# Kernel tuning notes

Hardware: AMD Instinct MI355X
Metric: run time of the kernel (lower is better)

The kernel has to match this reference:

```python
import jax, jax.numpy as jnp
import numpy as np

N_SENT, N_DOC, G = 100000, 10000, 32

def _seg_mean_right(x, src, dst, n_dst):
    # DGL GraphConv(norm='right'): sum incoming messages / in_degree (clamped to 1)
    m = jax.ops.segment_sum(x[src], dst, num_segments=n_dst)
    deg = jax.ops.segment_sum(jnp.ones_like(dst, dtype=x.dtype), dst, num_segments=n_dst)
    return m / jnp.maximum(deg, 1.0)[:, None]

def _rel_layer(xs, xd, coeff, basis, loop_w, bias,
               src_ss, dst_ss, src_sd, dst_sd, src_ds, dst_ds):
    # WeightBasis: per-relation weight = sum_b coeff[r,b] * basis[b]
    W = jnp.einsum('rb,bio->rio', coeff, basis)  # [3, in, out]
    # rel 0: sent->doc, rel 1: doc->sent, rel 2: sent->sent; HeteroGraphConv sums per dst ntype
    h_doc = _seg_mean_right(xs, src_sd, dst_sd, N_DOC) @ W[0]
    h_sent = (_seg_mean_right(xd, src_ds, dst_ds, N_SENT) @ W[1]
              + _seg_mean_right(xs, src_ss, dst_ss, N_SENT) @ W[2])
    h_sent = jax.nn.relu(h_sent + xs @ loop_w + bias)
    h_doc = jax.nn.relu(h_doc + xd @ loop_w + bias)
    return h_sent, h_doc

def setup_inputs() -> dict:
    key = jax.random.key(0)
    ks = jax.random.split(key, 20)
    d_in, d_h, d_o = 768, 256, 128
    inp = {
        'x_sent': jax.random.normal(ks[0], (N_SENT, d_in), jnp.float32),
        'x_doc': jax.random.normal(ks[1], (N_DOC, d_in), jnp.float32),
        'coeff1': jax.random.normal(ks[2], (3, 2), jnp.float32),
        'basis1': jax.random.normal(ks[3], (2, d_in, d_h), jnp.float32) * 0.02,
        'loop_w1': jax.random.normal(ks[4], (d_in, d_h), jnp.float32) * 0.02,
        'bias1': jnp.zeros((d_h,), jnp.float32),
        'coeff2': jax.random.normal(ks[5], (3, 2), jnp.float32),
        'basis2': jax.random.normal(ks[6], (2, d_h, d_o), jnp.float32) * 0.05,
        'loop_w2': jax.random.normal(ks[7], (d_h, d_o), jnp.float32) * 0.05,
        'bias2': jnp.zeros((d_o,), jnp.float32),
        'w_score': jax.random.normal(ks[8], (d_o, 1), jnp.float32) * 0.05,
        'b_score': jnp.zeros((1,), jnp.float32),
        'src_ss': jax.random.randint(ks[9], (400000,), 0, N_SENT, jnp.int32),
        'dst_ss': jax.random.randint(ks[10], (400000,), 0, N_SENT, jnp.int32),
        'src_sd': jax.random.randint(ks[11], (100000,), 0, N_SENT, jnp.int32),
        'dst_sd': jax.random.randint(ks[12], (100000,), 0, N_DOC, jnp.int32),
        'src_ds': jax.random.randint(ks[13], (100000,), 0, N_DOC, jnp.int32),
        'dst_ds': jax.random.randint(ks[14], (100000,), 0, N_SENT, jnp.int32),
        'gid_sent': jnp.sort(jax.random.randint(ks[15], (N_SENT,), 0, G, jnp.int32)),
        'gid_doc': jnp.sort(jax.random.randint(ks[16], (N_DOC,), 0, G, jnp.int32)),
        'num_graphs': G,
    }
    return inp

def reference(x_sent, x_doc, coeff1, basis1, loop_w1, bias1,
              coeff2, basis2, loop_w2, bias2, w_score, b_score,
              src_ss, dst_ss, src_sd, dst_sd, src_ds, dst_ds,
              gid_sent, gid_doc, num_graphs):
    h_s, h_d = _rel_layer(x_sent, x_doc, coeff1, basis1, loop_w1, bias1,
                          src_ss, dst_ss, src_sd, dst_sd, src_ds, dst_ds)
    h_s, h_d = _rel_layer(h_s, h_d, coeff2, basis2, loop_w2, bias2,
                          src_ss, dst_ss, src_sd, dst_sd, src_ds, dst_ds)
    # dgl.sum_nodes over batched graph, summed across ntypes
    readout = (jax.ops.segment_sum(h_s, gid_sent, num_segments=num_graphs)
               + jax.ops.segment_sum(h_d, gid_doc, num_segments=num_graphs))
    return readout @ w_score + b_score  # [G, 1]
```

## Files before the change

kernel.cpp:

```cpp
#include <hip/hip_runtime.h>

#define CDIV(a,b) (((a)+(b)-1)/(b))

typedef __attribute__((ext_vector_type(8))) short bf16x8;
typedef __attribute__((ext_vector_type(4))) float floatx4;

__device__ __forceinline__ ushort f2bf(float x) {
    unsigned u = __float_as_uint(x);
    return (ushort)((u + 0x7fffu + ((u >> 16) & 1u)) >> 16);
}
__device__ __forceinline__ float bflo(unsigned v) { return __uint_as_float(v << 16); }
__device__ __forceinline__ float bfhi(unsigned v) { return __uint_as_float(v & 0xffff0000u); }

__device__ __forceinline__ void load_lds16(const ushort* g, ushort* l) {
    __builtin_amdgcn_global_load_lds(
        (const __attribute__((address_space(1))) void*)g,
        (__attribute__((address_space(3))) void*)l, 16, 0, 0);
}


__global__ void zero_f4(float4* __restrict__ p, long long n4) {
    long long i = blockIdx.x * 256LL + threadIdx.x;
    if (i < n4) p[i] = make_float4(0.f, 0.f, 0.f, 0.f);
}

__global__ void fill_w5(ushort* __restrict__ BsT, ushort* __restrict__ BdT,
                        const float* __restrict__ basis, const float* __restrict__ loopw,
                        const float* __restrict__ coeff, int K, int N, long long KN) {
    long long i = blockIdx.x * 256LL + threadIdx.x;
    if (i >= KN) return;
    int k = (int)(i % K), n = (int)(i / K);
    int sec = blockIdx.y;
    float val;
    if (sec == 2 || sec == 4) {
        val = loopw[(size_t)k * N + n];
    } else {
        int r = (sec == 0) ? 0 : (sec == 1) ? 2 : 1;
        val = coeff[2 * r] * basis[(size_t)k * N + n] + coeff[2 * r + 1] * basis[KN + (size_t)k * N + n];
    }
    ushort* dst = (sec < 3) ? BsT : BdT;
    int col0 = (sec == 0) ? 0 : (sec == 1) ? N : (sec == 2) ? 2 * N : (sec == 3) ? 0 : N;
    dst[(size_t)(col0 + n) * K + k] = f2bf(val);
}


__global__ void accum_deg_all(const int* __restrict__ dss, const int* __restrict__ dds,
                              const int* __restrict__ dsd, int nss, int nds, int nsd,
                              int NS, int* __restrict__ deg) {
    int i = blockIdx.x * 256 + threadIdx.x;
    if (i < nss) atomicAdd(&deg[dss[i]], 1);
    else if (i < nss + nds) atomicAdd(&deg[NS + dds[i - nss]], 1);
    else if (i < nss + nds + nsd) atomicAdd(&deg[2 * NS + dsd[i - nss - nds]], 1);
}

__global__ void scan_p1(const int* __restrict__ deg, int n, int* __restrict__ bsum) {
    __shared__ int sd[256];
    int blk = blockIdx.x, tid = threadIdx.x;
    int i0 = blk * 1024 + tid * 4;
    int s = 0;
#pragma unroll
    for (int j = 0; j < 4; ++j) if (i0 + j < n) s += deg[i0 + j];
    sd[tid] = s; __syncthreads();
    for (int o = 128; o; o >>= 1) {
        if (tid < o) sd[tid] += sd[tid + o];
        __syncthreads();
    }
    if (tid == 0) bsum[blk] = sd[0];
}

__global__ void scan_p2(int* __restrict__ bsum, int nb, int* __restrict__ rowptr, int ntot, int etot) {
    __shared__ int sd[256];
    int tid = threadIdx.x;
    int v = (tid < nb) ? bsum[tid] : 0;
    sd[tid] = v; __syncthreads();
    for (int o = 1; o < 256; o <<= 1) {
        int t = (tid >= o) ? sd[tid - o] : 0;
        __syncthreads();
        sd[tid] += t;
        __syncthreads();
    }
    if (tid < nb) bsum[tid] = sd[tid] - v;
    if (tid == 0) rowptr[ntot] = etot;
}

__global__ void scan_p3(const int* __restrict__ deg, int n, const int* __restrict__ bsum,
                        int* __restrict__ rowptr) {
    __shared__ int sd[256];
    int blk = blockIdx.x, tid = threadIdx.x;
    int i0 = blk * 1024 + tid * 4;
    int v[4]; int s = 0;
#pragma unroll
    for (int j = 0; j < 4; ++j) { v[j] = (i0 + j < n) ? deg[i0 + j] : 0; s += v[j]; }
    sd[tid] = s; __syncthreads();
    for (int o = 1; o < 256; o <<= 1) {
        int t = (tid >= o) ? sd[tid - o] : 0;
        __syncthreads();
        sd[tid] += t;
        __syncthreads();
    }
    int excl = bsum[blk] + sd[tid] - s;
#pragma unroll
    for (int j = 0; j < 4; ++j) {
        if (i0 + j < n) rowptr[i0 + j] = excl;
        excl += v[j];
    }
}

__global__ void fill_csr_all(const int* __restrict__ sss, const int* __restrict__ dss,
                             const int* __restrict__ sds, const int* __restrict__ dds,
                             const int* __restrict__ ssd, const int* __restrict__ dsd,
                             int nss, int nds, int nsd, int NS,
                             const int* __restrict__ rowptr, int* __restrict__ fill,
                             int* __restrict__ col) {
    int i = blockIdx.x * 256 + threadIdx.x;
    int d, s;
    if (i < nss) { d = dss[i]; s = sss[i]; }
    else if (i < nss + nds) { int j = i - nss; d = NS + dds[j]; s = sds[j]; }
    else if (i < nss + nds + nsd) { int j = i - nss - nds; d = 2 * NS + dsd[j]; s = ssd[j]; }
    else return;
    int p = rowptr[d] + atomicAdd(&fill[d], 1);
    col[p] = s;
}

template<bool AF32>
__global__ __launch_bounds__(256) void gemm_any(
    const void* __restrict__ Araw, const ushort* __restrict__ Bt, ushort* __restrict__ C,
    int M, int K, int N, int BNX) {
    const int nwg = gridDim.x;
    const int orig = blockIdx.x;
    const int q = nwg >> 3, r = nwg & 7;
    const int xcd = orig & 7, idx = orig >> 3;
    const int wg = (xcd < r ? xcd * (q + 1) : r * (q + 1) + (xcd - r) * q) + idx;
    const int bn = (wg % BNX) * 128;
    const long long bm = (long long)(wg / BNX) * 128LL;

    __shared__ ushort As[128 * 32];
    __shared__ ushort Bs[128 * 32];
    const int tid = threadIdx.x;
    const int lane = tid & 63, wave = tid >> 6;
    const int mo = (wave & 1) * 64, no = (wave >> 1) * 64;
    const int l15 = lane & 15, quad = lane >> 4;
    const int srow0 = wave * 16 + (lane >> 2);
    const int schunk = (lane & 3) * 8;
    floatx4 acc[4][4] = {};

    for (int k0 = 0; k0 < K; k0 += 32) {
#pragma unroll
        for (int t = 0; t < 2; ++t) {
            int row = t * 64 + srow0;
            long long ar = bm + row; if (ar >= M) ar = M - 1;
            if (AF32) {
                const float* A = (const float*)Araw;
                const float* ap = A + ar * (size_t)K + k0 + schunk;
                float4 a0 = *(const float4*)ap;
                float4 a1 = *(const float4*)(ap + 4);
                uint4 o;
                o.x = (unsigned)f2bf(a0.x) | ((unsigned)f2bf(a0.y) << 16);
                o.y = (unsigned)f2bf(a0.z) | ((unsigned)f2bf(a0.w) << 16);
                o.z = (unsigned)f2bf(a1.x) | ((unsigned)f2bf(a1.y) << 16);
                o.w = (unsigned)f2bf(a1.z) | ((unsigned)f2bf(a1.w) << 16);
                *(uint4*)(As + t * 2048 + wave * 512 + lane * 8) = o;
            } else {
                load_lds16((const ushort*)Araw + ar * (size_t)K + k0 + schunk,
                           As + t * 2048 + wave * 512);
            }
            load_lds16(Bt + (size_t)(bn + row) * K + k0 + schunk, Bs + t * 2048 + wave * 512);
        }
        __syncthreads();
        bf16x8 af[4], bfr[4];
#pragma unroll
        for (int mt = 0; mt < 4; ++mt)
            af[mt] = *(const bf16x8*)(As + (mo + mt * 16 + l15) * 32 + quad * 8);
#pragma unroll
        for (int nt = 0; nt < 4; ++nt)
            bfr[nt] = *(const bf16x8*)(Bs + (no + nt * 16 + l15) * 32 + quad * 8);
#pragma unroll
        for (int mt = 0; mt < 4; ++mt)
#pragma unroll
            for (int nt = 0; nt < 4; ++nt)
                acc[mt][nt] = __builtin_amdgcn_mfma_f32_16x16x32_bf16(af[mt], bfr[nt], acc[mt][nt], 0, 0, 0);
        __syncthreads();
    }
#pragma unroll
    for (int mt = 0; mt < 4; ++mt)
#pragma unroll
        for (int i = 0; i < 4; ++i) {
            long long row = bm + mo + mt * 16 + quad * 4 + i;
            if (row < M) {
#pragma unroll
                for (int nt = 0; nt < 4; ++nt)
                    C[row * (size_t)N + bn + no + nt * 16 + l15] = f2bf(acc[mt][nt][i]);
            }
        }
}


__global__ __launch_bounds__(256) void gather_l1(
    const ushort* __restrict__ ys, const ushort* __restrict__ yd,
    const int* __restrict__ rowptr, const int* __restrict__ col,
    const float* __restrict__ bias, ushort* __restrict__ h1s, ushort* __restrict__ h1d,
    int NS, int ND) {
    int d = blockIdx.x * 4 + (threadIdx.x >> 6);
    int lane = threadIdx.x & 63;
    int cb = lane * 4;
    float b0 = bias[cb], b1 = bias[cb + 1], b2 = bias[cb + 2], b3 = bias[cb + 3];
    if (d < NS) {
        float a0 = 0, a1 = 0, a2 = 0, a3 = 0;
        int s0 = rowptr[d], s1 = rowptr[d + 1];
        int e = s0;
        for (; e + 4 <= s1; e += 4) {
            int sA = col[e], sB = col[e + 1], sC = col[e + 2], sD = col[e + 3];
            uint2 vA = *(const uint2*)(ys + (size_t)sA * 768 + 256 + cb);
            uint2 vB = *(const uint2*)(ys + (size_t)sB * 768 + 256 + cb);
            uint2 vC = *(const uint2*)(ys + (size_t)sC * 768 + 256 + cb);
            uint2 vD = *(const uint2*)(ys + (size_t)sD * 768 + 256 + cb);
            a0 += bflo(vA.x) + bflo(vB.x) + bflo(vC.x) + bflo(vD.x);
            a1 += bfhi(vA.x) + bfhi(vB.x) + bfhi(vC.x) + bfhi(vD.x);
            a2 += bflo(vA.y) + bflo(vB.y) + bflo(vC.y) + bflo(vD.y);
            a3 += bfhi(vA.y) + bfhi(vB.y) + bfhi(vC.y) + bfhi(vD.y);
        }
        for (; e < s1; ++e) {
            int s = col[e];
            uint2 v = *(const uint2*)(ys + (size_t)s * 768 + 256 + cb);
            a0 += bflo(v.x); a1 += bfhi(v.x); a2 += bflo(v.y); a3 += bfhi(v.y);
        }
        float inv = 1.f / (float)max(s1 - s0, 1);
        float m0 = a0 * inv, m1 = a1 * inv, m2 = a2 * inv, m3 = a3 * inv;
        a0 = a1 = a2 = a3 = 0.f;
        int t0 = rowptr[NS + d], t1 = rowptr[NS + d + 1];
        for (e = t0; e < t1; ++e) {
            int s = col[e];
            uint2 v = *(const uint2*)(yd + (size_t)s * 512 + cb);
            a0 += bflo(v.x); a1 += bfhi(v.x); a2 += bflo(v.y); a3 += bfhi(v.y);
        }
        inv = 1.f / (float)max(t1 - t0, 1);
        uint2 lv = *(const uint2*)(ys + (size_t)d * 768 + 512 + cb);
        float h0 = fmaxf(m0 + a0 * inv + bflo(lv.x) + b0, 0.f);
        float h1 = fmaxf(m1 + a1 * inv + bfhi(lv.x) + b1, 0.f);
        float h2 = fmaxf(m2 + a2 * inv + bflo(lv.y) + b2, 0.f);
        float h3 = fmaxf(m3 + a3 * inv + bfhi(lv.y) + b3, 0.f);
        uint2 o;
        o.x = (unsigned)f2bf(h0) | ((unsigned)f2bf(h1) << 16);
        o.y = (unsigned)f2bf(h2) | ((unsigned)f2bf(h3) << 16);
        *(uint2*)(h1s + (size_t)d * 256 + cb) = o;
    } else if (d < NS + ND) {
        int dd = d - NS;
        float a0 = 0, a1 = 0, a2 = 0, a3 = 0;
        int s0 = rowptr[2 * NS + dd], s1 = rowptr[2 * NS + dd + 1];
        int e = s0;
        for (; e + 4 <= s1; e += 4) {
            int sA = col[e], sB = col[e + 1], sC = col[e + 2], sD = col[e + 3];
            uint2 vA = *(const uint2*)(ys + (size_t)sA * 768 + cb);
            uint2 vB = *(const uint2*)(ys + (size_t)sB * 768 + cb);
            uint2 vC = *(const uint2*)(ys + (size_t)sC * 768 + cb);
            uint2 vD = *(const uint2*)(ys + (size_t)sD * 768 + cb);
            a0 += bflo(vA.x) + bflo(vB.x) + bflo(vC.x) + bflo(vD.x);
            a1 += bfhi(vA.x) + bfhi(vB.x) + bfhi(vC.x) + bfhi(vD.x);
            a2 += bflo(vA.y) + bflo(vB.y) + bflo(vC.y) + bflo(vD.y);
            a3 += bfhi(vA.y) + bfhi(vB.y) + bfhi(vC.y) + bfhi(vD.y);
        }
        for (; e < s1; ++e) {
            int s = col[e];
            uint2 v = *(const uint2*)(ys + (size_t)s * 768 + cb);
            a0 += bflo(v.x); a1 += bfhi(v.x); a2 += bflo(v.y); a3 += bfhi(v.y);
        }
        float inv = 1.f / (float)max(s1 - s0, 1);
        uint2 lv = *(const uint2*)(yd + (size_t)dd * 512 + 256 + cb);
        float h0 = fmaxf(a0 * inv + bflo(lv.x) + b0, 0.f);
        float h1 = fmaxf(a1 * inv + bfhi(lv.x) + b1, 0.f);
        float h2 = fmaxf(a2 * inv + bflo(lv.y) + b2, 0.f);
        float h3 = fmaxf(a3 * inv + bfhi(lv.y) + b3, 0.f);
        uint2 o;
        o.x = (unsigned)f2bf(h0) | ((unsigned)f2bf(h1) << 16);
        o.y = (unsigned)f2bf(h2) | ((unsigned)f2bf(h3) << 16);
        *(uint2*)(h1d + (size_t)dd * 256 + cb) = o;
    }
}

__global__ __launch_bounds__(256) void gather_l2(
    const ushort* __restrict__ ys, const ushort* __restrict__ yd,
    const int* __restrict__ rowptr, const int* __restrict__ col,
    const float* __restrict__ bias, const float* __restrict__ w,
    const int* __restrict__ gid_s, const int* __restrict__ gid_d,
    float* __restrict__ out, int NS, int ND, int G) {
    __shared__ float part[4][32];
    const int tid = threadIdx.x;
    const int lane = tid & 63, wv = tid >> 6;
    const int cb = lane * 2;
    const float w0 = w[cb], w1 = w[cb + 1];
    const float b0 = bias[cb], b1 = bias[cb + 1];
    float racc = 0.f;
    const int nw = gridDim.x * 4;
    for (int d = blockIdx.x * 4 + wv; d < NS + ND; d += nw) {
        float h0, h1; int g;
        if (d < NS) {
            float a0 = 0.f, a1 = 0.f;
            int s0 = rowptr[d], s1 = rowptr[d + 1];
            int e = s0;
            for (; e + 4 <= s1; e += 4) {
                int sA = col[e], sB = col[e + 1], sC = col[e + 2], sD = col[e + 3];
                unsigned vA = *(const unsigned*)(ys + (size_t)sA * 384 + 128 + cb);
                unsigned vB = *(const unsigned*)(ys + (size_t)sB * 384 + 128 + cb);
                unsigned vC = *(const unsigned*)(ys + (size_t)sC * 384 + 128 + cb);
                unsigned vD = *(const unsigned*)(ys + (size_t)sD * 384 + 128 + cb);
                a0 += bflo(vA) + bflo(vB) + bflo(vC) + bflo(vD);
                a1 += bfhi(vA) + bfhi(vB) + bfhi(vC) + bfhi(vD);
            }
            for (; e < s1; ++e) {
                int s = col[e];
                unsigned v = *(const unsigned*)(ys + (size_t)s * 384 + 128 + cb);
                a0 += bflo(v); a1 += bfhi(v);
            }
            float inv = 1.f / (float)max(s1 - s0, 1);
            float m0 = a0 * inv, m1 = a1 * inv;
            a0 = 0.f; a1 = 0.f;
            int t0 = rowptr[NS + d], t1 = rowptr[NS + d + 1];
            for (e = t0; e < t1; ++e) {
                int s = col[e];
                unsigned v = *(const unsigned*)(yd + (size_t)s * 256 + cb);
                a0 += bflo(v); a1 += bfhi(v);
            }
            inv = 1.f / (float)max(t1 - t0, 1);
            unsigned lv = *(const unsigned*)(ys + (size_t)d * 384 + 256 + cb);
            h0 = fmaxf(m0 + a0 * inv + bflo(lv) + b0, 0.f);
            h1 = fmaxf(m1 + a1 * inv + bfhi(lv) + b1, 0.f);
            g = gid_s[d];
        } else {
            int dd = d - NS;
            float a0 = 0.f, a1 = 0.f;
            int s0 = rowptr[2 * NS + dd], s1 = rowptr[2 * NS + dd + 1];
            int e = s0;
            for (; e + 4 <= s1; e += 4) {
                int sA = col[e], sB = col[e + 1], sC = col[e + 2], sD = col[e + 3];
                unsigned vA = *(const unsigned*)(ys + (size_t)sA * 384 + cb);
                unsigned vB = *(const unsigned*)(ys + (size_t)sB * 384 + cb);
                unsigned vC = *(const unsigned*)(ys + (size_t)sC * 384 + cb);
                unsigned vD = *(const unsigned*)(ys + (size_t)sD * 384 + cb);
                a0 += bflo(vA) + bflo(vB) + bflo(vC) + bflo(vD);
                a1 += bfhi(vA) + bfhi(vB) + bfhi(vC) + bfhi(vD);
            }
            for (; e < s1; ++e) {
                int s = col[e];
                unsigned v = *(const unsigned*)(ys + (size_t)s * 384 + cb);
                a0 += bflo(v); a1 += bfhi(v);
            }
            float inv = 1.f / (float)max(s1 - s0, 1);
            unsigned lv = *(const unsigned*)(yd + (size_t)dd * 256 + 128 + cb);
            h0 = fmaxf(a0 * inv + bflo(lv) + b0, 0.f);
            h1 = fmaxf(a1 * inv + bfhi(lv) + b1, 0.f);
            g = gid_d[dd];
        }
        float sc = h0 * w0 + h1 * w1;
#pragma unroll
        for (int o = 32; o; o >>= 1) sc += __shfl_down(sc, o);
        sc = __shfl(sc, 0);
        if (lane == g) racc += sc;
    }
    if (lane < 32) part[wv][lane] = racc;
    __syncthreads();
    if (tid < G) atomicAdd(&out[tid], part[0][tid] + part[1][tid] + part[2][tid] + part[3][tid]);
}

__global__ void init_out(float* __restrict__ out, const float* __restrict__ b, int G) {
    int i = threadIdx.x;
    if (i < G) out[i] = b[0];
}


extern "C" void kernel_launch(void* const* d_in, const int* in_sizes, int n_in,
                              void* d_out, int out_size, void* d_ws, size_t ws_size,
                              hipStream_t stream) {
    const float* x_sent = (const float*)d_in[0];
    const float* x_doc  = (const float*)d_in[1];
    const float* coeff1 = (const float*)d_in[2];
    const float* basis1 = (const float*)d_in[3];
    const float* loopw1 = (const float*)d_in[4];
    const float* bias1  = (const float*)d_in[5];
    const float* coeff2 = (const float*)d_in[6];
    const float* basis2 = (const float*)d_in[7];
    const float* loopw2 = (const float*)d_in[8];
    const float* bias2  = (const float*)d_in[9];
    const float* wscore = (const float*)d_in[10];
    const float* bscore = (const float*)d_in[11];
    const int* src_ss = (const int*)d_in[12];
    const int* dst_ss = (const int*)d_in[13];
    const int* src_sd = (const int*)d_in[14];
    const int* dst_sd = (const int*)d_in[15];
    const int* src_ds = (const int*)d_in[16];
    const int* dst_ds = (const int*)d_in[17];
    const int* gid_sent = (const int*)d_in[18];
    const int* gid_doc  = (const int*)d_in[19];

    const int DIN = 768, DH = 256, DOo = 128;
    const int NS = in_sizes[0] / DIN;
    const int ND = in_sizes[1] / DIN;
    const int E_SS = in_sizes[12], E_SD = in_sizes[14], E_DS = in_sizes[16];
    const int NTOT = NS + NS + ND;
    const int ETOT = E_SS + E_DS + E_SD;
    const int G = out_size;
    float* out = (float*)d_out;

    char* base = (char*)d_ws;
    size_t off = 0;
    auto alloc = [&](size_t bytes) -> char* {
        char* p = base + off;
        off = (off + bytes + 255) & ~(size_t)255;
        return p;
    };
    ushort* B1sT = (ushort*)alloc((size_t)768 * 768 * 2);
    ushort* B1dT = (ushort*)alloc((size_t)512 * 768 * 2);
    ushort* B2sT = (ushort*)alloc((size_t)384 * 256 * 2);
    ushort* B2dT = (ushort*)alloc((size_t)256 * 256 * 2);
    ushort* ys1 = (ushort*)alloc((size_t)NS * 768 * 2);
    ushort* yd1 = (ushort*)alloc((size_t)ND * 512 * 2);
    ushort* h1s = (ushort*)alloc((size_t)NS * 256 * 2);
    ushort* h1d = (ushort*)alloc((size_t)ND * 256 * 2);
    ushort* ys2 = (ushort*)alloc((size_t)NS * 384 * 2);
    ushort* yd2 = (ushort*)alloc((size_t)ND * 256 * 2);
    int* deg  = (int*)alloc((size_t)2 * NTOT * 4);
    int* fill = deg + NTOT;
    int* rowptr = (int*)alloc((size_t)(NTOT + 1) * 4);
    int* bsum = (int*)alloc(256 * 4);
    int* colall = (int*)alloc((size_t)ETOT * 4);

    long long t1 = (long long)768 * DH, t2 = (long long)256 * DOo;
    fill_w5<<<dim3((unsigned)CDIV(t1, 256), 5), 256, 0, stream>>>(B1sT, B1dT, basis1, loopw1, coeff1, 768, DH, t1);
    fill_w5<<<dim3((unsigned)CDIV(t2, 256), 5), 256, 0, stream>>>(B2sT, B2dT, basis2, loopw2, coeff2, 256, DOo, t2);

    zero_f4<<<(int)CDIV(2 * NTOT / 4, 256), 256, 0, stream>>>((float4*)deg, 2 * NTOT / 4);
    accum_deg_all<<<CDIV(ETOT, 256), 256, 0, stream>>>(dst_ss, dst_ds, dst_sd, E_SS, E_DS, E_SD, NS, deg);
    int nb = CDIV(NTOT, 1024);
    scan_p1<<<nb, 256, 0, stream>>>(deg, NTOT, bsum);
    scan_p2<<<1, 256, 0, stream>>>(bsum, nb, rowptr, NTOT, ETOT);
    scan_p3<<<nb, 256, 0, stream>>>(deg, NTOT, bsum, rowptr);
    fill_csr_all<<<CDIV(ETOT, 256), 256, 0, stream>>>(src_ss, dst_ss, src_ds, dst_ds, src_sd, dst_sd,
                                                      E_SS, E_DS, E_SD, NS, rowptr, fill, colall);

    {
        int mb = CDIV(NS, 128), mb0 = mb / 2;
        int M0 = mb0 * 128;
        gemm_any<true><<<6 * mb0, 256, 0, stream>>>(x_sent, B1sT, ys1, M0, 768, 768, 6);
        gemm_any<true><<<6 * (mb - mb0), 256, 0, stream>>>(
            x_sent + (size_t)M0 * 768, B1sT, ys1 + (size_t)M0 * 768, NS - M0, 768, 768, 6);
    }
    gemm_any<true><<<4 * CDIV(ND, 128), 256, 0, stream>>>(x_doc, B1dT, yd1, ND, 768, 512, 4);

    gather_l1<<<CDIV(NS + ND, 4), 256, 0, stream>>>(ys1, yd1, rowptr, colall, bias1, h1s, h1d, NS, ND);

    gemm_any<false><<<3 * CDIV(NS, 128), 256, 0, stream>>>(h1s, B2sT, ys2, NS, 256, 384, 3);
    gemm_any<false><<<2 * CDIV(ND, 128), 256, 0, stream>>>(h1d, B2dT, yd2, ND, 256, 256, 2);

    init_out<<<1, 64, 0, stream>>>(out, bscore, G);
    gather_l2<<<1100, 256, 0, stream>>>(ys2, yd2, rowptr, colall, bias2, wscore,
                                        gid_sent, gid_doc, out, NS, ND, G);
}
```

Baseline: 1.011 ms.

## Double-buffer LDS tiles in GEMM to overlap global loads with MFMA

Splits the GEMM's A and B shared-memory tiles into two buffers and prefetches the next K-slice while the MFMAs run on the current one. For fp32 A inputs, the next slice is held in registers and converted to bf16 into the alternate buffer after the compute step. This cuts one barrier per iteration and hides global-load latency. In exchange it doubles LDS use and adds prefetch registers, which may lower occupancy.

After: 1.045 ms. 3.4% more time.

```diff
diff --git a/kernel.cpp b/kernel.cpp
--- a/kernel.cpp
+++ b/kernel.cpp
@@ -134,8 +134,8 @@
     const int bn = (wg % BNX) * 128;
     const long long bm = (long long)(wg / BNX) * 128LL;
 
-    __shared__ ushort As[128 * 32];
-    __shared__ ushort Bs[128 * 32];
+    __shared__ ushort As[2][128 * 32];
+    __shared__ ushort Bs[2][128 * 32];
     const int tid = threadIdx.x;
     const int lane = tid & 63, wave = tid >> 6;
     const int mo = (wave & 1) * 64, no = (wave >> 1) * 64;
@@ -143,43 +143,75 @@
     const int srow0 = wave * 16 + (lane >> 2);
     const int schunk = (lane & 3) * 8;
     floatx4 acc[4][4] = {};
-
-    for (int k0 = 0; k0 < K; k0 += 32) {
+    float4 pre[2][2];
+
+    auto stageB = [&](int k0, int buf) {
+#pragma unroll
+        for (int t = 0; t < 2; ++t) {
+            int row = t * 64 + srow0;
+            load_lds16(Bt + (size_t)(bn + row) * K + k0 + schunk,
+                       Bs[buf] + t * 2048 + wave * 512);
+        }
+    };
+    auto stageA_bf16 = [&](int k0, int buf) {
 #pragma unroll
         for (int t = 0; t < 2; ++t) {
             int row = t * 64 + srow0;
             long long ar = bm + row; if (ar >= M) ar = M - 1;
-            if (AF32) {
-                const float* A = (const float*)Araw;
-                const float* ap = A + ar * (size_t)K + k0 + schunk;
-                float4 a0 = *(const float4*)ap;
-                float4 a1 = *(const float4*)(ap + 4);
-                uint4 o;
-                o.x = (unsigned)f2bf(a0.x) | ((unsigned)f2bf(a0.y) << 16);
-                o.y = (unsigned)f2bf(a0.z) | ((unsigned)f2bf(a0.w) << 16);
-                o.z = (unsigned)f2bf(a1.x) | ((unsigned)f2bf(a1.y) << 16);
-                o.w = (unsigned)f2bf(a1.z) | ((unsigned)f2bf(a1.w) << 16);
-                *(uint4*)(As + t * 2048 + wave * 512 + lane * 8) = o;
-            } else {
-                load_lds16((const ushort*)Araw + ar * (size_t)K + k0 + schunk,
-                           As + t * 2048 + wave * 512);
-            }
-            load_lds16(Bt + (size_t)(bn + row) * K + k0 + schunk, Bs + t * 2048 + wave * 512);
-        }
-        __syncthreads();
+            load_lds16((const ushort*)Araw + ar * (size_t)K + k0 + schunk,
+                       As[buf] + t * 2048 + wave * 512);
+        }
+    };
+    auto loadA_f32 = [&](int k0) {
+#pragma unroll
+        for (int t = 0; t < 2; ++t) {
+            int row = t * 64 + srow0;
+            long long ar = bm + row; if (ar >= M) ar = M - 1;
+            const float* ap = (const float*)Araw + ar * (size_t)K + k0 + schunk;
+            pre[t][0] = *(const float4*)ap;
+            pre[t][1] = *(const float4*)(ap + 4);
+        }
+    };
+    auto writeA = [&](int buf) {
+#pragma unroll
+        for (int t = 0; t < 2; ++t) {
+            uint4 o;
+            o.x = (unsigned)f2bf(pre[t][0].x) | ((unsigned)f2bf(pre[t][0].y) << 16);
+            o.y = (unsigned)f2bf(pre[t][0].z) | ((unsigned)f2bf(pre[t][0].w) << 16);
+            o.z = (unsigned)f2bf(pre[t][1].x) | ((unsigned)f2bf(pre[t][1].y) << 16);
+            o.w = (unsigned)f2bf(pre[t][1].z) | ((unsigned)f2bf(pre[t][1].w) << 16);
+            *(uint4*)(As[buf] + t * 2048 + wave * 512 + lane * 8) = o;
+        }
+    };
+
+    if (AF32) { loadA_f32(0); writeA(0); } else { stageA_bf16(0, 0); }
+    stageB(0, 0);
+    __syncthreads();
+
+    int cur = 0;
+    for (int k0 = 0; k0 < K; k0 += 32) {
+        const int nxt = k0 + 32;
+        const bool has = nxt < K;
+        if (has) {
+            if (AF32) loadA_f32(nxt);
+            else      stageA_bf16(nxt, cur ^ 1);
+            stageB(nxt, cur ^ 1);
+        }
         bf16x8 af[4], bfr[4];
 #pragma unroll
         for (int mt = 0; mt < 4; ++mt)
-            af[mt] = *(const bf16x8*)(As + (mo + mt * 16 + l15) * 32 + quad * 8);
+            af[mt] = *(const bf16x8*)(As[cur] + (mo + mt * 16 + l15) * 32 + quad * 8);
 #pragma unroll
         for (int nt = 0; nt < 4; ++nt)
-            bfr[nt] = *(const bf16x8*)(Bs + (no + nt * 16 + l15) * 32 + quad * 8);
+            bfr[nt] = *(const bf16x8*)(Bs[cur] + (no + nt * 16 + l15) * 32 + quad * 8);
 #pragma unroll
         for (int mt = 0; mt < 4; ++mt)
 #pragma unroll
             for (int nt = 0; nt < 4; ++nt)
                 acc[mt][nt] = __builtin_amdgcn_mfma_f32_16x16x32_bf16(af[mt], bfr[nt], acc[mt][nt], 0, 0, 0);
-        __syncthreads();
+        if (has && AF32) writeA(cur ^ 1);
+        __syncthreads();
+        cur ^= 1;
     }
 #pragma unroll
     for (int mt = 0; mt < 4; ++mt)
```

## Use BK=64 GEMM tiles with XOR-swizzled LDS layout pre-applied in global buffers

Applied to the files above, without the earlier changes.

The GEMM K-step grows from 32 to 64, and the shared-memory tiles use an XOR swizzle on 8-element chunks, keyed by row, to avoid LDS bank conflicts on the MFMA fragment reads. Because global_load_lds copies rows linearly, the swizzle is applied when the data is produced: the weight fill kernel and the layer-1 gather outputs write in swizzled order. The fp32 A path now issues all its global loads before converting them to bf16. This halves the barrier count per K and cuts bank conflicts, at the cost of double the LDS footprint and a swizzled storage format that every consumer of these buffers must respect.

Result: faster. 982.0 us (-2.9%).

```diff
diff --git a/kernel.cpp b/kernel.cpp
--- a/kernel.cpp
+++ b/kernel.cpp
@@ -17,6 +17,7 @@
         (const __attribute__((address_space(1))) void*)g,
         (__attribute__((address_space(3))) void*)l, 16, 0, 0);
 }
+
 
 
 __global__ void zero_f4(float4* __restrict__ p, long long n4) {
@@ -40,7 +41,8 @@
     }
     ushort* dst = (sec < 3) ? BsT : BdT;
     int col0 = (sec == 0) ? 0 : (sec == 1) ? N : (sec == 2) ? 2 * N : (sec == 3) ? 0 : N;
-    dst[(size_t)(col0 + n) * K + k] = f2bf(val);
+    int nn = col0 + n;
+    dst[(size_t)nn * K + (k & ~63) + ((k & 63) ^ ((nn & 7) << 3))] = f2bf(val);
 }
 
 
@@ -134,51 +136,76 @@
     const int bn = (wg % BNX) * 128;
     const long long bm = (long long)(wg / BNX) * 128LL;
 
-    __shared__ ushort As[128 * 32];
-    __shared__ ushort Bs[128 * 32];
+    __shared__ ushort As[128 * 64];
+    __shared__ ushort Bs[128 * 64];
     const int tid = threadIdx.x;
     const int lane = tid & 63, wave = tid >> 6;
     const int mo = (wave & 1) * 64, no = (wave >> 1) * 64;
     const int l15 = lane & 15, quad = lane >> 4;
-    const int srow0 = wave * 16 + (lane >> 2);
-    const int schunk = (lane & 3) * 8;
+    const int srow = wave * 8 + (lane >> 3);
+    const int bch = (lane & 7) * 8;
     floatx4 acc[4][4] = {};
 
-    for (int k0 = 0; k0 < K; k0 += 32) {
-#pragma unroll
-        for (int t = 0; t < 2; ++t) {
-            int row = t * 64 + srow0;
-            long long ar = bm + row; if (ar >= M) ar = M - 1;
-            if (AF32) {
-                const float* A = (const float*)Araw;
-                const float* ap = A + ar * (size_t)K + k0 + schunk;
-                float4 a0 = *(const float4*)ap;
-                float4 a1 = *(const float4*)(ap + 4);
+    for (int k0 = 0; k0 < K; k0 += 64) {
+#pragma unroll
+        for (int t = 0; t < 4; ++t) {
+            int row = t * 32 + srow;
+            load_lds16(Bt + (size_t)(bn + row) * K + k0 + bch,
+                       Bs + (t * 32 + wave * 8) * 64);
+        }
+        if (AF32) {
+            float4 pre[4][2];
+#pragma unroll
+            for (int j = 0; j < 4; ++j) {
+                int s = j * 256 + tid;
+                int arow = s >> 3, ach = s & 7;
+                long long ar = bm + arow; if (ar >= M) ar = M - 1;
+                const float* ap = (const float*)Araw + ar * (size_t)K + k0 + ach * 8;
+                pre[j][0] = *(const float4*)ap;
+                pre[j][1] = *(const float4*)(ap + 4);
+            }
+#pragma unroll
+            for (int j = 0; j < 4; ++j) {
+                int s = j * 256 + tid;
+                int arow = s >> 3, ach = s & 7;
                 uint4 o;
-                o.x = (unsigned)f2bf(a0.x) | ((unsigned)f2bf(a0.y) << 16);
-                o.y = (unsigned)f2bf(a0.z) | ((unsigned)f2bf(a0.w) << 16);
-                o.z = (unsigned)f2bf(a1.x) | ((unsigned)f2bf(a1.y) << 16);
-                o.w = (unsigned)f2bf(a1.z) | ((unsigned)f2bf(a1.w) << 16);
-                *(uint4*)(As + t * 2048 + wave * 512 + lane * 8) = o;
-            } else {
-                load_lds16((const ushort*)Araw + ar * (size_t)K + k0 + schunk,
-                           As + t * 2048 + wave * 512);
-            }
-            load_lds16(Bt + (size_t)(bn + row) * K + k0 + schunk, Bs + t * 2048 + wave * 512);
-        }
-        __syncthreads();
-        bf16x8 af[4], bfr[4];
-#pragma unroll
-        for (int mt = 0; mt < 4; ++mt)
-            af[mt] = *(const bf16x8*)(As + (mo + mt * 16 + l15) * 32 + quad * 8);
-#pragma unroll
-        for (int nt = 0; nt < 4; ++nt)
-            bfr[nt] = *(const bf16x8*)(Bs + (no + nt * 16 + l15) * 32 + quad * 8);
-#pragma unroll
-        for (int mt = 0; mt < 4; ++mt)
-#pragma unroll
-            for (int nt = 0; nt < 4; ++nt)
-                acc[mt][nt] = __builtin_amdgcn_mfma_f32_16x16x32_bf16(af[mt], bfr[nt], acc[mt][nt], 0, 0, 0);
+                o.x = (unsigned)f2bf(pre[j][0].x) | ((unsigned)f2bf(pre[j][0].y) << 16);
+                o.y = (unsigned)f2bf(pre[j][0].z) | ((unsigned)f2bf(pre[j][0].w) << 16);
+                o.z = (unsigned)f2bf(pre[j][1].x) | ((unsigned)f2bf(pre[j][1].y) << 16);
+                o.w = (unsigned)f2bf(pre[j][1].z) | ((unsigned)f2bf(pre[j][1].w) << 16);
+                *(uint4*)(As + arow * 64 + ((ach * 8) ^ ((arow & 7) << 3))) = o;
+            }
+        } else {
+#pragma unroll
+            for (int t = 0; t < 4; ++t) {
+                int row = t * 32 + srow;
+                long long ar = bm + row; if (ar >= M) ar = M - 1;
+                load_lds16((const ushort*)Araw + ar * (size_t)K + k0 + bch,
+                           As + (t * 32 + wave * 8) * 64);
+            }
+        }
+        __syncthreads();
+        bf16x8 af[2][4], bfr[2][4];
+#pragma unroll
+        for (int h = 0; h < 2; ++h) {
+#pragma unroll
+            for (int mt = 0; mt < 4; ++mt) {
+                int row = mo + mt * 16 + l15;
+                af[h][mt] = *(const bf16x8*)(As + row * 64 + ((h * 32 + quad * 8) ^ ((row & 7) << 3)));
+            }
+#pragma unroll
+            for (int nt = 0; nt < 4; ++nt) {
+                int row = no + nt * 16 + l15;
+                bfr[h][nt] = *(const bf16x8*)(Bs + row * 64 + ((h * 32 + quad * 8) ^ ((row & 7) << 3)));
+            }
+        }
+#pragma unroll
+        for (int h = 0; h < 2; ++h)
+#pragma unroll
+            for (int mt = 0; mt < 4; ++mt)
+#pragma unroll
+                for (int nt = 0; nt < 4; ++nt)
+                    acc[mt][nt] = __builtin_amdgcn_mfma_f32_16x16x32_bf16(af[h][mt], bfr[h][nt], acc[mt][nt], 0, 0, 0);
         __syncthreads();
     }
 #pragma unroll
@@ -242,7 +269,8 @@
         uint2 o;
         o.x = (unsigned)f2bf(h0) | ((unsigned)f2bf(h1) << 16);
         o.y = (unsigned)f2bf(h2) | ((unsigned)f2bf(h3) << 16);
-        *(uint2*)(h1s + (size_t)d * 256 + cb) = o;
+        int pos = (cb & ~63) + ((cb & 63) ^ ((d & 7) << 3));
+        *(uint2*)(h1s + (size_t)d * 256 + pos) = o;
     } else if (d < NS + ND) {
         int dd = d - NS;
         float a0 = 0, a1 = 0, a2 = 0, a3 = 0;
@@ -273,7 +301,8 @@
         uint2 o;
         o.x = (unsigned)f2bf(h0) | ((unsigned)f2bf(h1) << 16);
         o.y = (unsigned)f2bf(h2) | ((unsigned)f2bf(h3) << 16);
-        *(uint2*)(h1d + (size_t)dd * 256 + cb) = o;
+        int pos = (cb & ~63) + ((cb & 63) ^ ((dd & 7) << 3));
+        *(uint2*)(h1d + (size_t)dd * 256 + pos) = o;
     }
 }
 
```
